# Optimization experiments

Hardware: AMD Instinct MI355X
Metric: run time of the kernel (lower is better)

## Reference

```python
import jax, jax.numpy as jnp
from jax import lax
import numpy as np

B, N, C = 4, 2000, 80           # images, proposals/img, foreground classes
SCORE_THR = 0.05
IOU_THR = 0.5
MAX_PER_IMG = 100
K_PRE = 2000                     # pre-NMS top-k candidates per image
STDS = np.array([0.1, 0.1, 0.2, 0.2], dtype=np.float32)
MAX_RATIO = float(abs(np.log(16.0 / 1000.0)))  # wh_ratio_clip=16/1000


def setup_inputs() -> dict:
    key = jax.random.key(0)
    k1, k2, k3 = jax.random.split(key, 3)
    class_outs = jax.random.normal(k1, (B, N, C + 1), dtype=jnp.float32)
    regression_outs = jax.random.normal(k2, (B, N, C * 4), dtype=jnp.float32) * 0.5
    # random valid proposal boxes inside 800x1333 images (x1<x2, y1<y2)
    xy = jax.random.uniform(k3, (B, N, 2, 2), dtype=jnp.float32)
    xy = xy * jnp.array([1333.0, 800.0], dtype=jnp.float32)
    lo = jnp.min(xy, axis=2)
    hi = jnp.max(xy, axis=2) + 1.0
    boxes = jnp.concatenate([lo, hi], axis=-1)  # [B,N,4] x1,y1,x2,y2
    images_hw = jnp.tile(jnp.array([[800, 1333]], dtype=jnp.int32), (B, 1))
    return {"class_outs": class_outs, "regression_outs": regression_outs,
            "boxes": boxes, "images_hw": images_hw}


def _decode(props, deltas, h, w):
    # props [N,4], deltas [N,C,4] -> decoded boxes [N,C,4], clipped to image
    d = deltas * jnp.asarray(STDS)
    dx, dy, dw, dh = d[..., 0], d[..., 1], d[..., 2], d[..., 3]
    dw = jnp.clip(dw, -MAX_RATIO, MAX_RATIO)
    dh = jnp.clip(dh, -MAX_RATIO, MAX_RATIO)
    px = (props[:, None, 0] + props[:, None, 2]) * 0.5
    py = (props[:, None, 1] + props[:, None, 3]) * 0.5
    pw = props[:, None, 2] - props[:, None, 0]
    ph = props[:, None, 3] - props[:, None, 1]
    gx = px + pw * dx
    gy = py + ph * dy
    gw = pw * jnp.exp(dw)
    gh = ph * jnp.exp(dh)
    x1 = jnp.clip(gx - gw * 0.5, 0.0, w)
    y1 = jnp.clip(gy - gh * 0.5, 0.0, h)
    x2 = jnp.clip(gx + gw * 0.5, 0.0, w)
    y2 = jnp.clip(gy + gh * 0.5, 0.0, h)
    return jnp.stack([x1, y1, x2, y2], axis=-1)


def _pairwise_iou(b):
    # b [K,4] -> iou [K,K]
    area = (b[:, 2] - b[:, 0]) * (b[:, 3] - b[:, 1])
    lt = jnp.maximum(b[:, None, :2], b[None, :, :2])
    rb = jnp.minimum(b[:, None, 2:], b[None, :, 2:])
    wh = jnp.clip(rb - lt, 0.0)
    inter = wh[..., 0] * wh[..., 1]
    return inter / (area[:, None] + area[None, :] - inter + 1e-6)


def _process_image(cls_out, reg_out, props, hw):
    h = hw[0].astype(jnp.float32)
    w = hw[1].astype(jnp.float32)
    scores = jax.nn.softmax(cls_out, axis=-1)[:, :C]          # drop background col
    bboxes = _decode(props, reg_out.reshape(N, C, 4), h, w)   # [N,C,4]
    flat_scores = scores.reshape(-1)                          # [N*C]
    flat_boxes = bboxes.reshape(-1, 4)
    labels = jnp.tile(jnp.arange(C, dtype=jnp.int32), N)      # class fastest-varying
    cand = jnp.where(flat_scores > SCORE_THR, flat_scores, -1.0)
    top_scores, top_idx = lax.top_k(cand, K_PRE)
    top_boxes = flat_boxes[top_idx]
    top_labels = labels[top_idx]
    valid = top_scores > SCORE_THR
    # class-offset trick: boxes of distinct classes never overlap
    off = top_labels.astype(jnp.float32)[:, None] * (jnp.maximum(h, w) + 1.0)
    iou = _pairwise_iou(top_boxes + off)                      # [K_PRE,K_PRE]
    idxs = jnp.arange(K_PRE)

    def body(i, keep):
        sup = (idxs > i) & (iou[i] > IOU_THR) & keep[i]
        return keep & ~sup

    keep = lax.fori_loop(0, K_PRE, body, valid)
    kept_scores = jnp.where(keep, top_scores, -1.0)
    det_scores, det_i = lax.top_k(kept_scores, MAX_PER_IMG)
    det_valid = det_scores > SCORE_THR
    det_boxes = jnp.where(det_valid[:, None], top_boxes[det_i], 0.0)
    det_labels = jnp.where(det_valid, top_labels[det_i], -1)
    det_scores = jnp.where(det_valid, det_scores, 0.0)
    return det_boxes, det_scores, det_labels


def reference(class_outs, regression_outs, boxes, images_hw):
    det_boxes, det_scores, det_labels = jax.vmap(_process_image)(
        class_outs, regression_outs, boxes, images_hw)
    return det_boxes, det_scores, det_labels
```

## Files before the change

### kernel.cpp

```cpp
#include <hip/hip_runtime.h>


typedef unsigned long long u64;
typedef unsigned int u32;

#define B_ 4
#define N_ 2000
#define C_ 80
#define NCLS 81
#define KPRE 2000
#define MAXDET 100
#define TARGET 256
#define NB 2312
#define NBPAD 2368
#define NG 37
#define HBASE 0xF500
#define KSHIFT 46
#define CAPA 320
#define CAPB 2048
#define CAPBLK 128
#define BPI 125
#define BIGI 0x7fffffff

#define WS_GCNT  0
#define WS_GKEYS 2048
#define WS_GFLAG 514048
#define WS_GTHR  514064
#define WS_GHIST 514112

__device__ __forceinline__ u64 pack_key(float score, unsigned fi) {
  return ((u64)__float_as_uint(score) << 32) | (u64)(0xFFFFFFFFu - fi);
}
__device__ __forceinline__ int bucket_of_bits(u32 sb) {
  return min(max((int)(sb >> 14) - HBASE, 0), NB - 1);
}

__device__ __forceinline__ float wred_max(float v) {
  int t;
#define STEPM(ctrl)                                                          \
  t = __builtin_amdgcn_update_dpp(__float_as_int(v), __float_as_int(v),      \
                                  (ctrl), 0xF, 0xF, false);                  \
  v = fmaxf(v, __int_as_float(t));
  STEPM(0x111) STEPM(0x112) STEPM(0x114) STEPM(0x118) STEPM(0x142) STEPM(0x143)
#undef STEPM
  return __int_as_float(__builtin_amdgcn_readlane(__float_as_int(v), 63));
}
__device__ __forceinline__ float wred_sum(float v) {
  int t;
#define STEPS(ctrl)                                                          \
  t = __builtin_amdgcn_update_dpp(0, __float_as_int(v), (ctrl), 0xF, 0xF,    \
                                  false);                                    \
  v = v + __int_as_float(t);
  STEPS(0x111) STEPS(0x112) STEPS(0x114) STEPS(0x118) STEPS(0x142) STEPS(0x143)
#undef STEPS
  return __int_as_float(__builtin_amdgcn_readlane(__float_as_int(v), 63));
}

__device__ __forceinline__ int dpp_min8(int v) {
  int t;
  t = __builtin_amdgcn_update_dpp(BIGI, v, 0x104, 0xF, 0xF, false);
  v = min(v, t);
  t = __builtin_amdgcn_update_dpp(BIGI, v, 0x102, 0xF, 0xF, false);
  v = min(v, t);
  t = __builtin_amdgcn_update_dpp(BIGI, v, 0x101, 0xF, 0xF, false);
  v = min(v, t);
  return v;
}

__device__ __forceinline__ float4 decode_one(
    u64 kk, const float* __restrict__ reg, const float* __restrict__ props,
    int b, float h, float w, float offscale) {
  const float MAXR = 4.135166556742356f;
  unsigned fi = 0xFFFFFFFFu - (u32)kk;
  int n = (int)(fi / (unsigned)C_);
  int c = (int)(fi - (unsigned)n * (unsigned)C_);
  float4 p = ((const float4*)props)[b * N_ + n];
  const float* dl = reg + ((size_t)(b * N_ + n)) * (C_ * 4) + c * 4;
  float dx = dl[0] * 0.1f;
  float dy = dl[1] * 0.1f;
  float dw = fminf(fmaxf(dl[2] * 0.2f, -MAXR), MAXR);
  float dh = fminf(fmaxf(dl[3] * 0.2f, -MAXR), MAXR);
  float px = (p.x + p.z) * 0.5f, py = (p.y + p.w) * 0.5f;
  float pw = p.z - p.x, ph = p.w - p.y;
  float gx = px + pw * dx, gy = py + ph * dy;
  float gw = pw * expf(dw), gh = ph * expf(dh);
  float off = (float)c * offscale;
  return make_float4(fminf(fmaxf(gx - gw * 0.5f, 0.0f), w) + off,
                     fminf(fmaxf(gy - gh * 0.5f, 0.0f), h) + off,
                     fminf(fmaxf(gx + gw * 0.5f, 0.0f), w) + off,
                     fminf(fmaxf(gy + gh * 0.5f, 0.0f), h) + off);
}

__global__ __launch_bounds__(1024) void cand_kernel(
    const float* __restrict__ cls, u64* __restrict__ gkeys,
    int* __restrict__ gcnt, u32* __restrict__ ghist) {
  __shared__ int s_wc[16], s_woff[16];
  const int tid = threadIdx.x;
  const int w = tid >> 6, lane = tid & 63;
  const int blk = blockIdx.x;
  const int b = blk / BPI;
  const int n = (blk % BPI) * 16 + w;
  const float* lg = cls + (size_t)(b * N_ + n) * NCLS;
  float x0 = lg[lane];
  float x1 = (lane < 17) ? lg[64 + lane] : -3.0e38f;
  float mx = wred_max(fmaxf(x0, x1));
  float e0 = expf(x0 - mx);
  float e1 = (lane < 17) ? expf(x1 - mx) : 0.0f;
  float sum = wred_sum(e0 + e1);
  float sc0 = e0 / sum, sc1 = e1 / sum;
  bool p0 = sc0 > 0.05f;
  bool p1 = (lane < 16) && (sc1 > 0.05f);
  u64 m0 = __ballot(p0), m1 = __ballot(p1);
  int c0 = __popcll(m0);
  if (lane == 0) s_wc[w] = c0 + __popcll(m1);
  __syncthreads();
  if (tid == 0) {
    int acc = 0;
#pragma unroll
    for (int i = 0; i < 16; ++i) { s_woff[i] = acc; acc += s_wc[i]; }
    gcnt[blk] = acc;
  }
  __syncthreads();
  const int base = s_woff[w];
  const u64 lt = (1ull << lane) - 1;
  u64* gk = gkeys + (size_t)blk * CAPBLK;
  u32* gh = ghist + (size_t)b * NBPAD;
  if (p0) {
    int slot = base + __popcll(m0 & lt);
    if (slot < CAPBLK) gk[slot] = pack_key(sc0, (unsigned)(n * C_ + lane));
    atomicAdd(&gh[bucket_of_bits(__float_as_uint(sc0))], 1u);
  }
  if (p1) {
    int slot = base + c0 + __popcll(m1 & lt);
    if (slot < CAPBLK) gk[slot] = pack_key(sc1, (unsigned)(n * C_ + 64 + lane));
    atomicAdd(&gh[bucket_of_bits(__float_as_uint(sc1))], 1u);
  }
}

__global__ __launch_bounds__(1024) void thresh_kernel(
    const u32* __restrict__ ghist, int* __restrict__ gthr) {
  __shared__ u32 hist[NBPAD];
  __shared__ int s_coarse[64];
  const int b = blockIdx.x, tid = threadIdx.x;
  const int wv = tid >> 6, lane = tid & 63;
  for (int i = tid; i < NBPAD; i += 1024) hist[i] = ghist[b * NBPAD + i];
  if (tid < 64) s_coarse[tid] = 0;
  __syncthreads();
  for (int g2 = wv; g2 < NG; g2 += 16) {
    int v = (int)hist[(g2 << 6) | lane];
#pragma unroll
    for (int o = 32; o; o >>= 1) v += __shfl_xor(v, o);
    if (lane == 0) s_coarse[g2] = v;
  }
  __syncthreads();
  if (tid < 64) {
    int v = s_coarse[lane];
#pragma unroll
    for (int off = 1; off < 64; off <<= 1) {
      int src = lane + off;
      int o = __shfl(v, src < 64 ? src : 63);
      if (src < 64) v += o;
    }
    int Mtot = __shfl(v, 0);
    u64 pm = __ballot(v >= TARGET);
    int T_A = 0, S_A;
    if (pm) {
      int gs = 63 - __builtin_clzll(pm);
      int beyond = __shfl(v, gs + 1);
      int fv = (int)hist[(gs << 6) | lane];
#pragma unroll
      for (int off = 1; off < 64; off <<= 1) {
        int src = lane + off;
        int o = __shfl(fv, src < 64 ? src : 63);
        if (src < 64) fv += o;
      }
      int cum = beyond + fv;
      u64 pm2 = __ballot(cum >= TARGET);
      int tr = 63 - __builtin_clzll(pm2);
      T_A = (gs << 6) + tr;
      S_A = __shfl(cum, tr);
    } else {
      S_A = Mtot;
    }
    if (lane == 0) {
      gthr[b * 4 + 0] = T_A;
      gthr[b * 4 + 1] = S_A;
      gthr[b * 4 + 2] = Mtot;
    }
  }
}

__global__ __launch_bounds__(1024) void nmsA_kernel(
    const float* __restrict__ reg, const float* __restrict__ props,
    const int* __restrict__ hw, const u64* __restrict__ gkeys,
    const int* __restrict__ gcnt, const int* __restrict__ gthr,
    int* __restrict__ gflag, float* __restrict__ out) {
  __shared__ u64 lds8[4106];
  char* bp = (char*)lds8;
  u64* SS = (u64*)bp;
  u64* rb = (u64*)(bp + 4096);
  float4* bxA = (float4*)(bp + 24576);
  u64* U = (u64*)(bp + 29696);
  int* outl = (int*)(bp + 32272);
  int* misc = (int*)(bp + 32784);

  const int b = blockIdx.x, tid = threadIdx.x;
  const int wv = tid >> 6, lane = tid & 63;

  float h = (float)hw[b * 2 + 0];
  float w = (float)hw[b * 2 + 1];
  float offscale = fmaxf(h, w) + 1.0f;
  const int T_A = gthr[b * 4 + 0];
  const int S_A = gthr[b * 4 + 1];
  const int Mtot = gthr[b * 4 + 2];

  if (tid < 16) misc[tid] = 0;
  __syncthreads();

  bool modeB = (S_A > CAPA);
  int K = 0, nkept = 0;

  if (!modeB) {
    int cnts[8];
#pragma unroll
    for (int k = 0; k < 8; k++) {
      int p = wv + 16 * k;
      cnts[k] = (p < BPI) ? gcnt[b * BPI + p] : 0;
    }
    bool ovf = false;
#pragma unroll
    for (int k = 0; k < 8; k++) {
      int p = wv + 16 * k;
      if (p >= BPI) break;
      int cnt = cnts[k];
      if (cnt > CAPBLK) { ovf = true; cnt = CAPBLK; }
      const u64* seg = gkeys + (size_t)(b * BPI + p) * CAPBLK;
#pragma unroll
      for (int r = 0; r < 2; r++) {
        int idx = lane + 64 * r;
        bool pred = false;
        u64 key = 0;
        if (idx < cnt) {
          key = seg[idx];
          pred = (bucket_of_bits((u32)(key >> 32)) >= T_A);
        }
        u64 mk = __ballot(pred);
        if (mk) {
          int wbase = 0;
          if (lane == 0) wbase = atomicAdd(&misc[4], __popcll(mk));
          wbase = __shfl(wbase, 0);
          if (pred) {
            int pos = wbase + __popcll(mk & ((1ull << lane) - 1));
            if (pos < CAPA) U[pos] = key;
          }
        }
      }
    }
    if (lane == 0 && ovf) misc[7] = 1;
    __syncthreads();
    if (misc[7]) modeB = true;
    int S = misc[4];
    if (S > CAPA) S = CAPA;

    if (!modeB) {
      if (tid == 0 && (S & 1)) U[S] = 0ULL;
      __syncthreads();
      if (tid < S) {
        u64 k1 = U[tid];
        int r1 = 0;
        const ulonglong2* Uu2 = (const ulonglong2*)U;
        int half = (S + 1) >> 1;
        for (int k = 0; k < half; k++) {
          ulonglong2 kk = Uu2[k];
          r1 += (kk.x > k1) + (kk.y > k1);
        }
        SS[r1] = k1;
      }
      __syncthreads();
      K = S;
      for (int j = tid; j < K; j += 1024)
        bxA[j] = decode_one(SS[j], reg, props, b, h, w, offscale);
      __syncthreads();

      int nwords = (S + 63) >> 6;
      int ntiles = nwords * (nwords + 1) / 2;
      for (int t = wv; t < ntiles; t += 16) {
        int ti = 0, rem = t;
        while (rem >= nwords - ti) { rem -= nwords - ti; ti++; }
        int tj = ti + rem;
        int i = (ti << 6) + lane;
        float4 bi4 = bxA[i];
        float ai = (bi4.z - bi4.x) * (bi4.w - bi4.y);
        u64 bits = 0;
        int jbase = tj << 6;
        int jcount = min(64, S - jbase);
        for (int jj = 0; jj < jcount; jj++) {
          int j = jbase + jj;
          float4 bj = bxA[j];
          float aj = (bj.z - bj.x) * (bj.w - bj.y);
          float iw = fmaxf(fminf(bi4.z, bj.z) - fmaxf(bi4.x, bj.x), 0.0f);
          float ih = fmaxf(fminf(bi4.w, bj.w) - fmaxf(bi4.y, bj.y), 0.0f);
          float inter = iw * ih;
          float iou = inter / (ai + aj - inter + 1e-6f);
          if (j > i && iou > 0.5f) bits |= (1ull << jj);
        }
        if (i < S) rb[i * 8 + tj] = bits;
      }
      __syncthreads();

      if (tid < 64) {
        u64 alive = 0;
        if (lane < nwords) {
          alive = ~0ull;
          int remb = S & 63;
          if (lane == nwords - 1 && remb) alive = (1ull << remb) - 1;
        }
        int nk = 0;
        if (S > 0) {
          int i = 0;
          u64 row = (lane < nwords) ? rb[0 * 8 + lane] : 0ull;
          for (;;) {
            if (lane == 0) outl[nk] = i;
            nk++;
            if (nk >= MAXDET) break;
            if (lane == (i >> 6)) alive &= ~(1ull << (i & 63));
            u64 rowSpec = (i + 1 < S && lane < nwords) ? rb[(i + 1) * 8 + lane] : 0ull;
            u64 a2 = alive & ~row;
            alive = a2;
            int cnd = a2 ? ((lane << 6) + (int)__builtin_ctzll(a2)) : BIGI;
            int m8 = dpp_min8(cnd);
            int ni = __builtin_amdgcn_readfirstlane(m8);
            if (ni >= BIGI) break;
            row = (ni == i + 1) ? rowSpec
                                : ((lane < nwords) ? rb[ni * 8 + lane] : 0ull);
            i = ni;
          }
        }
        if (lane == 0) misc[6] = nk;
      }
      __syncthreads();
      nkept = misc[6];
      if (nkept < MAXDET && K < Mtot && K < KPRE) modeB = true;
    }
  }

  if (tid == 0) gflag[b] = modeB ? 1 : 0;
  if (modeB) return;

  float* oBox = out;
  float* oSc = out + B_ * MAXDET * 4;
  float* oLb = out + B_ * MAXDET * 5;
  for (int k2 = tid; k2 < MAXDET; k2 += 1024) {
    float4 bb = make_float4(0.0f, 0.0f, 0.0f, 0.0f);
    float sv = 0.0f, lv = -1.0f;
    if (k2 < nkept) {
      int idx = outl[k2];
      u64 kk = SS[idx];
      sv = __uint_as_float((u32)(kk >> 32));
      unsigned fi = 0xFFFFFFFFu - (u32)kk;
      int c = (int)(fi % (unsigned)C_);
      float off = (float)c * offscale;
      float4 ob = bxA[idx];
      bb = make_float4(ob.x - off, ob.y - off, ob.z - off, ob.w - off);
      lv = (float)c;
    }
    oBox[(b * MAXDET + k2) * 4 + 0] = bb.x;
    oBox[(b * MAXDET + k2) * 4 + 1] = bb.y;
    oBox[(b * MAXDET + k2) * 4 + 2] = bb.z;
    oBox[(b * MAXDET + k2) * 4 + 3] = bb.w;
    oSc[b * MAXDET + k2] = sv;
    oLb[b * MAXDET + k2] = lv;
  }
}

__global__ __launch_bounds__(1024) void nmsB_kernel(
    const float* __restrict__ reg, const float* __restrict__ props,
    const int* __restrict__ hw, const u64* __restrict__ gkeys,
    const int* __restrict__ gcnt, const int* __restrict__ gflag,
    float* __restrict__ out) {
  const int b = blockIdx.x, tid = threadIdx.x;
  if (gflag[b] == 0) return;

  __shared__ u64 lds8[7952];
  char* bp = (char*)lds8;
  u32* hist = (u32*)(bp + 0);
  u64* U2 = (u64*)(bp + 9472);
  u64* SSB = (u64*)(bp + 25856);
  int* outl = (int*)(bp + 42240);
  int* misc = (int*)(bp + 42752);
  const int wv = tid >> 6, lane = tid & 63;

  float h = (float)hw[b * 2 + 0];
  float w = (float)hw[b * 2 + 1];
  float offscale = fmaxf(h, w) + 1.0f;

  for (int i = tid; i < NBPAD; i += 1024) hist[i] = 0;
  if (tid < 16) misc[tid] = 0;
  __syncthreads();

  for (int k = 0; k < 8; k++) {
    int p = wv + 16 * k;
    if (p >= BPI) break;
    int cnt = min(gcnt[b * BPI + p], CAPBLK);
    const u64* seg = gkeys + (size_t)(b * BPI + p) * CAPBLK;
#pragma unroll
    for (int r = 0; r < 2; r++) {
      int idx = lane + 64 * r;
      if (idx < cnt) {
        u64 key = seg[idx];
        int bi = min(max((int)(key >> KSHIFT) - HBASE, 0), NB - 1);
        atomicAdd(&hist[bi], 1u);
      }
    }
  }
  __syncthreads();

  if (tid == 0) {
    int acc = 0, tb = 0;
    for (int bi = NB - 1; bi >= 0; bi--) {
      acc += (int)hist[bi];
      if (acc >= KPRE) { tb = bi; break; }
    }
    if (acc > CAPB) tb = min(tb + 1, NB - 1);
    misc[1] = tb;
    misc[4] = 0;
  }
  __syncthreads();
  int T_B = misc[1];

  for (int k = 0; k < 8; k++) {
    int p = wv + 16 * k;
    if (p >= BPI) break;
    int cnt = min(gcnt[b * BPI + p], CAPBLK);
    const u64* seg = gkeys + (size_t)(b * BPI + p) * CAPBLK;
#pragma unroll
    for (int r = 0; r < 2; r++) {
      int idx = lane + 64 * r;
      bool pred = false;
      u64 key = 0;
      if (idx < cnt) {
        key = seg[idx];
        int bi = min(max((int)(key >> KSHIFT) - HBASE, 0), NB - 1);
        pred = (bi >= T_B);
      }
      u64 mk = __ballot(pred);
      if (mk) {
        int wbase = 0;
        if (lane == 0) wbase = atomicAdd(&misc[4], __popcll(mk));
        wbase = __shfl(wbase, 0);
        if (pred) {
          int pos = wbase + __popcll(mk & ((1ull << lane) - 1));
          if (pos < CAPB) U2[pos] = key;
        }
      }
    }
  }
  __syncthreads();
  int S = misc[4];
  if (S > CAPB) S = CAPB;
  {
    int j1 = tid, j2 = tid + 1024;
    u64 k1 = (j1 < S) ? U2[j1] : 0ULL;
    u64 k2 = (j2 < S) ? U2[j2] : 0ULL;
    int r1 = 0, r2 = 0;
    for (int k = 0; k < S; k++) {
      u64 kk = U2[k];
      r1 += (kk > k1);
      r2 += (kk > k2);
    }
    __syncthreads();
    if (j1 < S) SSB[r1] = k1;
    if (j2 < S) SSB[r2] = k2;
  }
  __syncthreads();
  int K = (S < KPRE) ? S : KPRE;
  int j1 = tid, j2 = tid + 1024;
  bool kp1 = (j1 < K), kp2 = (j2 < K);
  float4 bb1 = kp1 ? decode_one(SSB[j1], reg, props, b, h, w, offscale)
                   : make_float4(0, 0, 0, 0);
  float4 bb2 = kp2 ? decode_one(SSB[j2], reg, props, b, h, w, offscale)
                   : make_float4(0, 0, 0, 0);
  int nk = 0;
  if (K > 0) {
    int i = 0;
    for (;;) {
      if (tid == 0) { outl[nk] = i; misc[5] = K; }
      nk++;
      if (nk >= MAXDET) break;
      __syncthreads();
      float4 tb = decode_one(SSB[i], reg, props, b, h, w, offscale);
      float ai = (tb.z - tb.x) * (tb.w - tb.y);
      int ln = K;
      if (kp1 && j1 > i) {
        float aj = (bb1.z - bb1.x) * (bb1.w - bb1.y);
        float iw = fmaxf(fminf(tb.z, bb1.z) - fmaxf(tb.x, bb1.x), 0.0f);
        float ih = fmaxf(fminf(tb.w, bb1.w) - fmaxf(tb.y, bb1.y), 0.0f);
        float inter = iw * ih;
        float iou = inter / (ai + aj - inter + 1e-6f);
        if (iou > 0.5f) kp1 = false;
        else ln = min(ln, j1);
      }
      if (kp2 && j2 > i) {
        float aj = (bb2.z - bb2.x) * (bb2.w - bb2.y);
        float iw = fmaxf(fminf(tb.z, bb2.z) - fmaxf(tb.x, bb2.x), 0.0f);
        float ih = fmaxf(fminf(tb.w, bb2.w) - fmaxf(tb.y, bb2.y), 0.0f);
        float inter = iw * ih;
        float iou = inter / (ai + aj - inter + 1e-6f);
        if (iou > 0.5f) kp2 = false;
        else ln = min(ln, j2);
      }
#pragma unroll
      for (int off = 32; off; off >>= 1) ln = min(ln, __shfl_xor(ln, off));
      if ((tid & 63) == 0 && ln < K) atomicMin(&misc[5], ln);
      __syncthreads();
      int ni = misc[5];
      __syncthreads();
      if (ni >= K) break;
      i = ni;
    }
  }
  if (tid == 0) misc[6] = nk;
  __syncthreads();
  int nkept = misc[6];

  float* oBox = out;
  float* oSc = out + B_ * MAXDET * 4;
  float* oLb = out + B_ * MAXDET * 5;
  for (int k2 = tid; k2 < MAXDET; k2 += 1024) {
    float4 bb = make_float4(0.0f, 0.0f, 0.0f, 0.0f);
    float sv = 0.0f, lv = -1.0f;
    if (k2 < nkept) {
      int idx = outl[k2];
      u64 kk = SSB[idx];
      sv = __uint_as_float((u32)(kk >> 32));
      unsigned fi = 0xFFFFFFFFu - (u32)kk;
      int c = (int)(fi % (unsigned)C_);
      float off = (float)c * offscale;
      float4 ob = decode_one(kk, reg, props, b, h, w, offscale);
      bb = make_float4(ob.x - off, ob.y - off, ob.z - off, ob.w - off);
      lv = (float)c;
    }
    oBox[(b * MAXDET + k2) * 4 + 0] = bb.x;
    oBox[(b * MAXDET + k2) * 4 + 1] = bb.y;
    oBox[(b * MAXDET + k2) * 4 + 2] = bb.z;
    oBox[(b * MAXDET + k2) * 4 + 3] = bb.w;
    oSc[b * MAXDET + k2] = sv;
    oLb[b * MAXDET + k2] = lv;
  }
}

extern "C" void kernel_launch(void* const* d_in, const int* in_sizes, int n_in,
                              void* d_out, int out_size, void* d_ws, size_t ws_size,
                              hipStream_t stream) {
  const float* cls = (const float*)d_in[0];
  const float* reg = (const float*)d_in[1];
  const float* props = (const float*)d_in[2];
  const int* hw = (const int*)d_in[3];
  float* out = (float*)d_out;

  int* gcnt = (int*)((char*)d_ws + WS_GCNT);
  u64* gkeys = (u64*)((char*)d_ws + WS_GKEYS);
  int* gflag = (int*)((char*)d_ws + WS_GFLAG);
  int* gthr = (int*)((char*)d_ws + WS_GTHR);
  u32* ghist = (u32*)((char*)d_ws + WS_GHIST);

  hipMemsetAsync(ghist, 0, (size_t)B_ * NBPAD * 4, stream);
  cand_kernel<<<B_ * BPI, 1024, 0, stream>>>(cls, gkeys, gcnt, ghist);
  thresh_kernel<<<B_, 1024, 0, stream>>>(ghist, gthr);
  nmsA_kernel<<<B_, 1024, 0, stream>>>(reg, props, hw, gkeys, gcnt, gthr,
                                       gflag, out);
  nmsB_kernel<<<B_, 1024, 0, stream>>>(reg, props, hw, gkeys, gcnt, gflag, out);
}
```

Before: 112.3 us.

## Fuse threshold kernel into NMS-A and prefetch candidate keys during histogram scan

Removes the separate threshold kernel and computes the histogram threshold inside nmsA, so one launch and a global round-trip through the threshold buffer go away. Fourteen waves prefetch the candidate keys into registers while two waves reduce the histogram, overlapping the key loads with the threshold computation. The fast-path capacity and target drop from 320/256 to 256/192, which shrinks the LDS footprint and the suppression bitmask rows. The catch is that more images may now fall back to the slower mode-B path when the candidate count exceeds the smaller capacity.

```diff
diff --git a/kernel.cpp b/kernel.cpp
--- a/kernel.cpp
+++ b/kernel.cpp
@@ -10,23 +10,23 @@
 #define NCLS 81
 #define KPRE 2000
 #define MAXDET 100
-#define TARGET 256
+#define TARGET 192
 #define NB 2312
 #define NBPAD 2368
 #define NG 37
 #define HBASE 0xF500
 #define KSHIFT 46
-#define CAPA 320
+#define CAPA 256
 #define CAPB 2048
 #define CAPBLK 128
 #define BPI 125
+#define SPW 9
 #define BIGI 0x7fffffff
 
 #define WS_GCNT  0
 #define WS_GKEYS 2048
 #define WS_GFLAG 514048
-#define WS_GTHR  514064
-#define WS_GHIST 514112
+#define WS_GHIST 514064
 
 __device__ __forceinline__ u64 pack_key(float score, unsigned fi) {
   return ((u64)__float_as_uint(score) << 32) | (u64)(0xFFFFFFFFu - fi);
@@ -137,22 +137,59 @@
   }
 }
 
-__global__ __launch_bounds__(1024) void thresh_kernel(
-    const u32* __restrict__ ghist, int* __restrict__ gthr) {
-  __shared__ u32 hist[NBPAD];
-  __shared__ int s_coarse[64];
+__global__ __launch_bounds__(1024) void nmsA_kernel(
+    const float* __restrict__ reg, const float* __restrict__ props,
+    const int* __restrict__ hw, const u64* __restrict__ gkeys,
+    const int* __restrict__ gcnt, const u32* __restrict__ ghist,
+    int* __restrict__ gflag, float* __restrict__ out) {
+  __shared__ u64 lds8[2156];
+  char* bp = (char*)lds8;
+  u64* SS = (u64*)bp;
+  u64* U = (u64*)(bp + 2048);
+  u64* rb = (u64*)(bp + 4128);
+  float4* bxA = (float4*)(bp + 12320);
+  int* outl = (int*)(bp + 16416);
+  int* misc = (int*)(bp + 16928);
+  int* s_coarse = (int*)(bp + 16992);
+
   const int b = blockIdx.x, tid = threadIdx.x;
   const int wv = tid >> 6, lane = tid & 63;
-  for (int i = tid; i < NBPAD; i += 1024) hist[i] = ghist[b * NBPAD + i];
-  if (tid < 64) s_coarse[tid] = 0;
-  __syncthreads();
-  for (int g2 = wv; g2 < NG; g2 += 16) {
-    int v = (int)hist[(g2 << 6) | lane];
-#pragma unroll
-    for (int o = 32; o; o >>= 1) v += __shfl_xor(v, o);
-    if (lane == 0) s_coarse[g2] = v;
-  }
-  __syncthreads();
+
+  float h = (float)hw[b * 2 + 0];
+  float w = (float)hw[b * 2 + 1];
+  float offscale = fmaxf(h, w) + 1.0f;
+
+  if (tid < 16) misc[tid] = 0;
+  if (tid >= NG && tid < 64) s_coarse[tid] = 0;
+
+  int cnts[SPW];
+  u64 ka[SPW], kb[SPW];
+  if (wv < 14) {
+#pragma unroll
+    for (int k = 0; k < SPW; k++) {
+      int p = wv * SPW + k;
+      cnts[k] = (p < BPI) ? gcnt[b * BPI + p] : 0;
+    }
+#pragma unroll
+    for (int k = 0; k < SPW; k++) {
+      int p = wv * SPW + k;
+      int cnt = min(cnts[k], CAPBLK);
+      const u64* seg = gkeys + (size_t)(b * BPI + p) * CAPBLK;
+      ka[k] = (lane < cnt) ? seg[lane] : 0ULL;
+      kb[k] = (64 + lane < cnt) ? seg[64 + lane] : 0ULL;
+    }
+  } else {
+    int g0 = (wv == 14) ? 0 : 19;
+    int g1 = (wv == 14) ? 19 : NG;
+    for (int g2 = g0; g2 < g1; g2++) {
+      int v = (int)ghist[b * NBPAD + ((g2 << 6) | lane)];
+#pragma unroll
+      for (int o = 32; o; o >>= 1) v += __shfl_xor(v, o);
+      if (lane == 0) s_coarse[g2] = v;
+    }
+  }
+  __syncthreads();
+
   if (tid < 64) {
     int v = s_coarse[lane];
 #pragma unroll
@@ -167,7 +204,7 @@
     if (pm) {
       int gs = 63 - __builtin_clzll(pm);
       int beyond = __shfl(v, gs + 1);
-      int fv = (int)hist[(gs << 6) | lane];
+      int fv = (int)ghist[b * NBPAD + ((gs << 6) | lane)];
 #pragma unroll
       for (int off = 1; off < 64; off <<= 1) {
         int src = lane + off;
@@ -182,81 +219,49 @@
     } else {
       S_A = Mtot;
     }
-    if (lane == 0) {
-      gthr[b * 4 + 0] = T_A;
-      gthr[b * 4 + 1] = S_A;
-      gthr[b * 4 + 2] = Mtot;
-    }
-  }
-}
-
-__global__ __launch_bounds__(1024) void nmsA_kernel(
-    const float* __restrict__ reg, const float* __restrict__ props,
-    const int* __restrict__ hw, const u64* __restrict__ gkeys,
-    const int* __restrict__ gcnt, const int* __restrict__ gthr,
-    int* __restrict__ gflag, float* __restrict__ out) {
-  __shared__ u64 lds8[4106];
-  char* bp = (char*)lds8;
-  u64* SS = (u64*)bp;
-  u64* rb = (u64*)(bp + 4096);
-  float4* bxA = (float4*)(bp + 24576);
-  u64* U = (u64*)(bp + 29696);
-  int* outl = (int*)(bp + 32272);
-  int* misc = (int*)(bp + 32784);
-
-  const int b = blockIdx.x, tid = threadIdx.x;
-  const int wv = tid >> 6, lane = tid & 63;
-
-  float h = (float)hw[b * 2 + 0];
-  float w = (float)hw[b * 2 + 1];
-  float offscale = fmaxf(h, w) + 1.0f;
-  const int T_A = gthr[b * 4 + 0];
-  const int S_A = gthr[b * 4 + 1];
-  const int Mtot = gthr[b * 4 + 2];
-
-  if (tid < 16) misc[tid] = 0;
-  __syncthreads();
-
+    if (lane == 0) { misc[0] = T_A; misc[2] = S_A; misc[3] = Mtot; }
+  }
+  __syncthreads();
+
+  const int T_A = misc[0], S_A = misc[2], Mtot = misc[3];
   bool modeB = (S_A > CAPA);
   int K = 0, nkept = 0;
 
   if (!modeB) {
-    int cnts[8];
-#pragma unroll
-    for (int k = 0; k < 8; k++) {
-      int p = wv + 16 * k;
-      cnts[k] = (p < BPI) ? gcnt[b * BPI + p] : 0;
-    }
-    bool ovf = false;
-#pragma unroll
-    for (int k = 0; k < 8; k++) {
-      int p = wv + 16 * k;
-      if (p >= BPI) break;
-      int cnt = cnts[k];
-      if (cnt > CAPBLK) { ovf = true; cnt = CAPBLK; }
-      const u64* seg = gkeys + (size_t)(b * BPI + p) * CAPBLK;
-#pragma unroll
-      for (int r = 0; r < 2; r++) {
-        int idx = lane + 64 * r;
-        bool pred = false;
-        u64 key = 0;
-        if (idx < cnt) {
-          key = seg[idx];
-          pred = (bucket_of_bits((u32)(key >> 32)) >= T_A);
-        }
-        u64 mk = __ballot(pred);
+    if (wv < 14) {
+      bool ovf = false;
+      const u64 lt = (1ull << lane) - 1;
+#pragma unroll
+      for (int k = 0; k < SPW; k++) {
+        int cnt = cnts[k];
+        if (cnt > CAPBLK) { ovf = true; cnt = CAPBLK; }
+        bool pr = (lane < cnt) &&
+                  (bucket_of_bits((u32)(ka[k] >> 32)) >= T_A);
+        u64 mk = __ballot(pr);
         if (mk) {
           int wbase = 0;
           if (lane == 0) wbase = atomicAdd(&misc[4], __popcll(mk));
           wbase = __shfl(wbase, 0);
-          if (pred) {
-            int pos = wbase + __popcll(mk & ((1ull << lane) - 1));
-            if (pos < CAPA) U[pos] = key;
+          if (pr) {
+            int pos = wbase + __popcll(mk & lt);
+            if (pos < CAPA) U[pos] = ka[k];
           }
         }
-      }
-    }
-    if (lane == 0 && ovf) misc[7] = 1;
+        pr = (64 + lane < cnt) &&
+             (bucket_of_bits((u32)(kb[k] >> 32)) >= T_A);
+        mk = __ballot(pr);
+        if (mk) {
+          int wbase = 0;
+          if (lane == 0) wbase = atomicAdd(&misc[4], __popcll(mk));
+          wbase = __shfl(wbase, 0);
+          if (pr) {
+            int pos = wbase + __popcll(mk & lt);
+            if (pos < CAPA) U[pos] = kb[k];
+          }
+        }
+      }
+      if (lane == 0 && ovf) misc[7] = 1;
+    }
     __syncthreads();
     if (misc[7]) modeB = true;
     int S = misc[4];
@@ -304,27 +309,28 @@
           float iou = inter / (ai + aj - inter + 1e-6f);
           if (j > i && iou > 0.5f) bits |= (1ull << jj);
         }
-        if (i < S) rb[i * 8 + tj] = bits;
+        if (i < S) rb[i * 4 + tj] = bits;
       }
       __syncthreads();
 
       if (tid < 64) {
+        int nw7 = (S + 63) >> 6;
         u64 alive = 0;
-        if (lane < nwords) {
+        if (lane < nw7) {
           alive = ~0ull;
           int remb = S & 63;
-          if (lane == nwords - 1 && remb) alive = (1ull << remb) - 1;
+          if (lane == nw7 - 1 && remb) alive = (1ull << remb) - 1;
         }
         int nk = 0;
         if (S > 0) {
           int i = 0;
-          u64 row = (lane < nwords) ? rb[0 * 8 + lane] : 0ull;
+          u64 row = (lane < nw7) ? rb[0 * 4 + lane] : 0ull;
           for (;;) {
             if (lane == 0) outl[nk] = i;
             nk++;
             if (nk >= MAXDET) break;
             if (lane == (i >> 6)) alive &= ~(1ull << (i & 63));
-            u64 rowSpec = (i + 1 < S && lane < nwords) ? rb[(i + 1) * 8 + lane] : 0ull;
+            u64 rowSpec = (i + 1 < S && lane < nw7) ? rb[(i + 1) * 4 + lane] : 0ull;
             u64 a2 = alive & ~row;
             alive = a2;
             int cnd = a2 ? ((lane << 6) + (int)__builtin_ctzll(a2)) : BIGI;
@@ -332,7 +338,7 @@
             int ni = __builtin_amdgcn_readfirstlane(m8);
             if (ni >= BIGI) break;
             row = (ni == i + 1) ? rowSpec
-                                : ((lane < nwords) ? rb[ni * 8 + lane] : 0ull);
+                                : ((lane < nw7) ? rb[ni * 4 + lane] : 0ull);
             i = ni;
           }
         }
@@ -561,13 +567,11 @@
   int* gcnt = (int*)((char*)d_ws + WS_GCNT);
   u64* gkeys = (u64*)((char*)d_ws + WS_GKEYS);
   int* gflag = (int*)((char*)d_ws + WS_GFLAG);
-  int* gthr = (int*)((char*)d_ws + WS_GTHR);
   u32* ghist = (u32*)((char*)d_ws + WS_GHIST);
 
   hipMemsetAsync(ghist, 0, (size_t)B_ * NBPAD * 4, stream);
   cand_kernel<<<B_ * BPI, 1024, 0, stream>>>(cls, gkeys, gcnt, ghist);
-  thresh_kernel<<<B_, 1024, 0, stream>>>(ghist, gthr);
-  nmsA_kernel<<<B_, 1024, 0, stream>>>(reg, props, hw, gkeys, gcnt, gthr,
+  nmsA_kernel<<<B_, 1024, 0, stream>>>(reg, props, hw, gkeys, gcnt, ghist,
                                        gflag, out);
   nmsB_kernel<<<B_, 1024, 0, stream>>>(reg, props, hw, gkeys, gcnt, gflag, out);
 }
```

After: 112.4 us. Within noise of the previous version (+0.1%).
